# Optimization experiments

Measured on AMD Instinct MI355X. Metric: run time of the kernel, lower is better.

## Reference

```python
import jax, jax.numpy as jnp
import numpy as np

N = 50000
E = 600000
F_IN = 128
HID = 128
N_CLS = 16


def setup_inputs() -> dict:
    key = jax.random.key(0)
    ks = jax.random.split(key, 12)
    x = jax.random.normal(ks[0], (N, F_IN), dtype=jnp.float32)
    edge_index = jax.random.randint(ks[1], (2, E), 0, N, dtype=jnp.int64)
    def glorot(k, shape):
        lim = float(np.sqrt(6.0 / (shape[0] + shape[1])))
        return jax.random.uniform(k, shape, jnp.float32, -lim, lim)
    return {
        "x": x,
        "edge_index": edge_index,
        "W1": glorot(ks[2], (F_IN, HID)), "b1": jnp.zeros((HID,), jnp.float32),
        "W2": glorot(ks[3], (HID, HID)), "b2": jnp.zeros((HID,), jnp.float32),
        "W3": glorot(ks[4], (HID, HID)), "b3": jnp.zeros((HID,), jnp.float32),
        "Wlin": glorot(ks[5], (HID, N_CLS)), "blin": jnp.zeros((N_CLS,), jnp.float32),
    }


def _gcn_norm(edge_index, n_nodes):
    # PyG GCNConv default: add self-loops, symmetric normalization
    loops = jnp.arange(n_nodes, dtype=edge_index.dtype)
    src = jnp.concatenate([edge_index[0], loops])  # [E+N]
    dst = jnp.concatenate([edge_index[1], loops])  # [E+N]
    deg = jax.ops.segment_sum(jnp.ones_like(dst, dtype=jnp.float32), dst,
                              num_segments=n_nodes)
    dis = jnp.where(deg > 0, jax.lax.rsqrt(jnp.maximum(deg, 1.0)), 0.0)
    norm = dis[src] * dis[dst]  # [E+N]
    return src, dst, norm


def _gcn_conv(h, src, dst, norm, n_nodes, W, b):
    h = h @ W                                   # transform first (small GEMM)
    msg = h[src] * norm[:, None]                # gather + scale, [E+N, HID]
    out = jax.ops.segment_sum(msg, dst, num_segments=n_nodes)  # scatter-add
    return out + b


def reference(x, edge_index, W1, b1, W2, b2, W3, b3, Wlin, blin):
    n_nodes = x.shape[0]
    src, dst, norm = _gcn_norm(edge_index, n_nodes)
    h = jax.nn.relu(_gcn_conv(x, src, dst, norm, n_nodes, W1, b1))
    h = jax.nn.relu(_gcn_conv(h, src, dst, norm, n_nodes, W2, b2))
    h = _gcn_conv(h, src, dst, norm, n_nodes, W3, b3)
    return h @ Wlin + blin  # [N, N_CLS]
```

## Files before the change

### kernel.cpp

```cpp
#include <hip/hip_runtime.h>
#include <hip/hip_fp16.h>


#define FD 128
#define NCLS 16

typedef _Float16 f16x8 __attribute__((ext_vector_type(8)));
typedef float f32x4 __attribute__((ext_vector_type(4)));

__global__ __launch_bounds__(256) void k_init_deg(int* __restrict__ degi, int n) {
  int i = blockIdx.x * 256 + threadIdx.x;
  if (i < n) degi[i] = 1;
}

__global__ __launch_bounds__(256) void k_count(const int* __restrict__ dst,
                                               int* __restrict__ degi, int e) {
  int i = blockIdx.x * 256 + threadIdx.x;
  if (i < e) atomicAdd(&degi[dst[i]], 1);
}

__global__ __launch_bounds__(1024) void k_scanA(const int* __restrict__ degi,
                                                int* __restrict__ ptr,
                                                int* __restrict__ bsum,
                                                float* __restrict__ dis, int n) {
  __shared__ int buf[1024];
  int tid = threadIdx.x;
  int i = blockIdx.x * 1024 + tid;
  int dg = (i < n) ? degi[i] : 1;
  if (i < n) dis[i] = rsqrtf((float)dg);
  int v = (i < n) ? (dg - 1) : 0;
  buf[tid] = v;
  __syncthreads();
  for (int off = 1; off < 1024; off <<= 1) {
    int t = (tid >= off) ? buf[tid - off] : 0;
    __syncthreads();
    buf[tid] += t;
    __syncthreads();
  }
  if (i < n) ptr[i] = buf[tid] - v;
  if (tid == 1023) bsum[blockIdx.x] = buf[1023];
}

__global__ void k_scanB(int* __restrict__ bsum, int nb) {
  if (threadIdx.x == 0 && blockIdx.x == 0) {
    int run = 0;
    for (int b = 0; b < nb; ++b) { int t = bsum[b]; bsum[b] = run; run += t; }
  }
}

__global__ __launch_bounds__(256) void k_scanC(int* __restrict__ ptr,
                                               int* __restrict__ cur,
                                               const int* __restrict__ bsum,
                                               int n, int e) {
  int i = blockIdx.x * 256 + threadIdx.x;
  if (i < n) {
    int p = ptr[i] + bsum[i >> 10];
    ptr[i] = p;
    cur[i] = p;
  }
  if (i == 0) ptr[n] = e;
}

__global__ __launch_bounds__(256) void k_fill(const int* __restrict__ src,
                                              const int* __restrict__ dst,
                                              int* __restrict__ cur,
                                              const float* __restrict__ dis,
                                              int2* __restrict__ sn, int e) {
  int i = blockIdx.x * 256 + threadIdx.x;
  if (i < e) {
    int s = src[i], d = dst[i];
    int p = atomicAdd(&cur[d], 1);
    sn[p] = make_int2(s, __float_as_int(dis[s] * dis[d]));
  }
}

__global__ __launch_bounds__(256) void k_convW3(const float* __restrict__ W1,
                                                const float* __restrict__ W2,
                                                const float* __restrict__ W3,
                                                __half* __restrict__ wp) {
  int gi = blockIdx.x * 256 + threadIdx.x;
  int which = gi >> 14;
  int i = gi & 16383;
  const float* W = (which == 0) ? W1 : ((which == 1) ? W2 : W3);
  int j = i & 7;
  int l = (i >> 3) & 63;
  int kc = (i >> 9) & 3;
  int c = i >> 11;
  int k = kc * 32 + ((l >> 4) << 3) + j;
  int col = c * 16 + (l & 15);
  wp[gi] = __float2half_rn(W[k * FD + col]);
}

__global__ __launch_bounds__(256) void k_gemm_mfma(const void* __restrict__ Ain,
                                                   int a_fp32,
                                                   const __half* __restrict__ Wp,
                                                   __half* __restrict__ C, int n) {
  __shared__ uint4 al4[1024];
  __shared__ uint4 wl4[2048];
  int tid = threadIdx.x;
  const uint4* wsrc = reinterpret_cast<const uint4*>(Wp);
  for (int i = tid; i < 2048; i += 256) wl4[i] = wsrc[i];

  int rb = blockIdx.x * 64;
  if (a_fp32) {
    const float* A = (const float*)Ain;
    for (int i = tid; i < 2048; i += 256) {
      int row = i >> 5, seg = i & 31;
      int g = rb + row;
      if (g > n - 1) g = n - 1;
      float4 v = *reinterpret_cast<const float4*>(A + (size_t)g * FD + seg * 4);
      __half h[4];
      h[0] = __float2half_rn(v.x); h[1] = __float2half_rn(v.y);
      h[2] = __float2half_rn(v.z); h[3] = __float2half_rn(v.w);
      *reinterpret_cast<uint2*>(reinterpret_cast<char*>(al4) + row * 256 +
                                ((seg * 8) ^ ((row & 7) << 4))) =
          *reinterpret_cast<uint2*>(h);
    }
  } else {
    const __half* A = (const __half*)Ain;
    for (int i = tid; i < 1024; i += 256) {
      int row = i >> 4, b = (i & 15) << 4;
      int g = rb + row;
      if (g > n - 1) g = n - 1;
      uint4 v = *reinterpret_cast<const uint4*>(
          reinterpret_cast<const char*>(A) + (size_t)g * 256 + b);
      *reinterpret_cast<uint4*>(reinterpret_cast<char*>(al4) + row * 256 +
                                (b ^ ((row & 7) << 4))) = v;
    }
  }
  __syncthreads();

  int l = tid & 63, wid = tid >> 6;
  int arow = wid * 16 + (l & 15);
  f16x8 af[4];
#pragma unroll
  for (int kc = 0; kc < 4; ++kc) {
    int b = kc * 64 + ((l >> 4) << 4);
    af[kc] = *reinterpret_cast<const f16x8*>(
        reinterpret_cast<const char*>(al4) + arow * 256 + (b ^ ((arow & 7) << 4)));
  }

  const __half* wl = reinterpret_cast<const __half*>(wl4);
  f32x4 acc[8];
#pragma unroll
  for (int c = 0; c < 8; ++c) acc[c] = (f32x4){0.f, 0.f, 0.f, 0.f};
#pragma unroll
  for (int c = 0; c < 8; ++c) {
#pragma unroll
    for (int kc = 0; kc < 4; ++kc) {
      f16x8 bf = *reinterpret_cast<const f16x8*>(&wl[((c * 4 + kc) * 64 + l) * 8]);
      acc[c] = __builtin_amdgcn_mfma_f32_16x16x32_f16(af[kc], bf, acc[c], 0, 0, 0);
    }
  }

  __syncthreads();
  {
    char* cl = reinterpret_cast<char*>(al4);
    int crow0 = wid * 16 + ((l >> 4) << 2);
#pragma unroll
    for (int c = 0; c < 8; ++c) {
      int colb = (c * 16 + (l & 15)) * 2;
#pragma unroll
      for (int r = 0; r < 4; ++r) {
        int row = crow0 + r;
        *reinterpret_cast<__half*>(cl + row * 256 + (colb ^ ((row & 7) << 4))) =
            __float2half_rn(acc[c][r]);
      }
    }
  }
  __syncthreads();
  for (int i = tid; i < 1024; i += 256) {
    int row = i >> 4, seg = i & 15;
    int g = rb + row;
    if (g < n)
      *reinterpret_cast<uint4*>(reinterpret_cast<char*>(C) + (size_t)g * 256 +
                                seg * 16) =
          *reinterpret_cast<const uint4*>(reinterpret_cast<const char*>(al4) +
                                          row * 256 +
                                          ((seg * 16) ^ ((row & 7) << 4)));
  }
}

__device__ __forceinline__ void agg_wave(const __half* __restrict__ t,
                                         const int* __restrict__ ptr,
                                         const int2* __restrict__ sn,
                                         int node, int lane, float o[4]) {
  int h = lane >> 5;
  int q = lane & 31;
  float a0 = 0.f, a1 = 0.f, a2 = 0.f, a3 = 0.f;
  int e0 = ptr[node], e1 = ptr[node + 1];
  for (int base = e0; base < e1; base += 16) {
    int s[8];
    float w[8];
#pragma unroll
    for (int j = 0; j < 8; ++j) {
      int idx = base + 2 * j + h;
      if (idx < e1) {
        int2 p = sn[idx];
        s[j] = p.x;
        w[j] = __int_as_float(p.y);
      } else {
        s[j] = node;
        w[j] = 0.f;
      }
    }
    ushort4 v[8];
#pragma unroll
    for (int j = 0; j < 8; ++j)
      v[j] = *reinterpret_cast<const ushort4*>(&t[(size_t)s[j] * FD + q * 4]);
#pragma unroll
    for (int j = 0; j < 8; ++j) {
      a0 = fmaf(__half2float(__ushort_as_half(v[j].x)), w[j], a0);
      a1 = fmaf(__half2float(__ushort_as_half(v[j].y)), w[j], a1);
      a2 = fmaf(__half2float(__ushort_as_half(v[j].z)), w[j], a2);
      a3 = fmaf(__half2float(__ushort_as_half(v[j].w)), w[j], a3);
    }
  }
  o[0] = a0 + __shfl(a0, lane ^ 32, 64);
  o[1] = a1 + __shfl(a1, lane ^ 32, 64);
  o[2] = a2 + __shfl(a2, lane ^ 32, 64);
  o[3] = a3 + __shfl(a3, lane ^ 32, 64);
}

template <int SELF>
__global__ __launch_bounds__(256) void k_probe(const __half* __restrict__ t,
                                               const int* __restrict__ ptr,
                                               const int2* __restrict__ sn,
                                               float* __restrict__ pr) {
  int lane = threadIdx.x & 63;
  int node = blockIdx.x * 4 + (threadIdx.x >> 6);
  int h = lane >> 5, q = lane & 31;
  float a0 = 0.f, a1 = 0.f, a2 = 0.f, a3 = 0.f;
  int e0 = ptr[node], e1 = ptr[node + 1];
  for (int base = e0; base < e1; base += 16) {
    int s[8];
    float w[8];
#pragma unroll
    for (int j = 0; j < 8; ++j) {
      int idx = base + 2 * j + h;
      if (idx < e1) {
        int2 p = sn[idx];
        s[j] = p.x;
        w[j] = __int_as_float(p.y);
      } else {
        s[j] = node;
        w[j] = 0.f;
      }
      if (SELF) {
        int nd = node;
        asm volatile("" : "+v"(nd));
        s[j] = nd;
      }
    }
    ushort4 v[8];
#pragma unroll
    for (int j = 0; j < 8; ++j)
      v[j] = *reinterpret_cast<const ushort4*>(&t[(size_t)s[j] * FD + q * 4]);
#pragma unroll
    for (int j = 0; j < 8; ++j) {
      a0 = fmaf(__half2float(__ushort_as_half(v[j].x)), w[j], a0);
      a1 = fmaf(__half2float(__ushort_as_half(v[j].y)), w[j], a1);
      a2 = fmaf(__half2float(__ushort_as_half(v[j].z)), w[j], a2);
      a3 = fmaf(__half2float(__ushort_as_half(v[j].w)), w[j], a3);
    }
  }
  a0 += __shfl(a0, lane ^ 32, 64);
  a1 += __shfl(a1, lane ^ 32, 64);
  a2 += __shfl(a2, lane ^ 32, 64);
  a3 += __shfl(a3, lane ^ 32, 64);
  if (lane < 32)
    *reinterpret_cast<float4*>(&pr[((size_t)node * 32 + q) * 4]) =
        make_float4(a0, a1, a2, a3);
}

__global__ __launch_bounds__(256) void k_agg(const __half* __restrict__ t,
                                             const int* __restrict__ ptr,
                                             const int2* __restrict__ sn,
                                             const float* __restrict__ dis,
                                             const float* __restrict__ bias,
                                             __half* __restrict__ out, int relu) {
  int lane = threadIdx.x & 63;
  int node = blockIdx.x * 4 + (threadIdx.x >> 6);
  float d = dis[node];
  float dd = d * d;
  float o[4];
  agg_wave(t, ptr, sn, node, lane, o);
  if (lane < 32) {
    int q = lane;
    ushort4 sv = *reinterpret_cast<const ushort4*>(&t[(size_t)node * FD + q * 4]);
    float4 b = *reinterpret_cast<const float4*>(&bias[q * 4]);
    o[0] = fmaf(__half2float(__ushort_as_half(sv.x)), dd, o[0]) + b.x;
    o[1] = fmaf(__half2float(__ushort_as_half(sv.y)), dd, o[1]) + b.y;
    o[2] = fmaf(__half2float(__ushort_as_half(sv.z)), dd, o[2]) + b.z;
    o[3] = fmaf(__half2float(__ushort_as_half(sv.w)), dd, o[3]) + b.w;
    if (relu) {
      o[0] = fmaxf(o[0], 0.f);
      o[1] = fmaxf(o[1], 0.f);
      o[2] = fmaxf(o[2], 0.f);
      o[3] = fmaxf(o[3], 0.f);
    }
    __half hh[4];
    hh[0] = __float2half_rn(o[0]);
    hh[1] = __float2half_rn(o[1]);
    hh[2] = __float2half_rn(o[2]);
    hh[3] = __float2half_rn(o[3]);
    *reinterpret_cast<uint2*>(&out[(size_t)node * FD + q * 4]) =
        *reinterpret_cast<uint2*>(hh);
  }
}

__global__ __launch_bounds__(256) void k_agg_lin(const __half* __restrict__ t,
                                                 const int* __restrict__ ptr,
                                                 const int2* __restrict__ sn,
                                                 const float* __restrict__ dis,
                                                 const float* __restrict__ b3,
                                                 const float* __restrict__ Wl,
                                                 const float* __restrict__ bl,
                                                 float* __restrict__ out) {
  __shared__ float hl[4][FD];
  int wid = threadIdx.x >> 6;
  int lane = threadIdx.x & 63;
  int node = blockIdx.x * 4 + wid;
  float d = dis[node];
  float dd = d * d;
  float o[4];
  agg_wave(t, ptr, sn, node, lane, o);
  if (lane < 32) {
    int q = lane;
    ushort4 sv = *reinterpret_cast<const ushort4*>(&t[(size_t)node * FD + q * 4]);
    float4 b = *reinterpret_cast<const float4*>(&b3[q * 4]);
    hl[wid][q * 4 + 0] = fmaf(__half2float(__ushort_as_half(sv.x)), dd, o[0]) + b.x;
    hl[wid][q * 4 + 1] = fmaf(__half2float(__ushort_as_half(sv.y)), dd, o[1]) + b.y;
    hl[wid][q * 4 + 2] = fmaf(__half2float(__ushort_as_half(sv.z)), dd, o[2]) + b.z;
    hl[wid][q * 4 + 3] = fmaf(__half2float(__ushort_as_half(sv.w)), dd, o[3]) + b.w;
  }
  __syncthreads();
  int c = lane & 15, kc = lane >> 4;
  float s = 0.f;
#pragma unroll
  for (int k0 = 0; k0 < 32; ++k0) {
    int k = kc * 32 + k0;
    s = fmaf(hl[wid][k], Wl[k * NCLS + c], s);
  }
  s += __shfl(s, lane ^ 16, 64);
  s += __shfl(s, lane ^ 32, 64);
  if (lane < NCLS)
    out[(size_t)node * NCLS + lane] = s + bl[lane];
}

extern "C" void kernel_launch(void* const* d_in, const int* in_sizes, int n_in,
                              void* d_out, int out_size, void* d_ws, size_t ws_size,
                              hipStream_t stream) {
  const float* x  = (const float*)d_in[0];
  const int*   ei = (const int*)d_in[1];
  const float* W1 = (const float*)d_in[2];
  const float* b1 = (const float*)d_in[3];
  const float* W2 = (const float*)d_in[4];
  const float* b2 = (const float*)d_in[5];
  const float* W3 = (const float*)d_in[6];
  const float* b3 = (const float*)d_in[7];
  const float* Wl = (const float*)d_in[8];
  const float* bl = (const float*)d_in[9];
  float* out = (float*)d_out;

  const int n = in_sizes[0] / FD;
  const int e = in_sizes[1] / 2;
  const int* src = ei;
  const int* dst = ei + e;

  __half* thA = (__half*)d_ws;
  __half* thB = thA + (size_t)n * FD;
  float*  pr  = (float*)(thB + (size_t)n * FD);
  __half* wp1 = (__half*)(pr + (size_t)n * FD);
  __half* wp2 = wp1 + 16384;
  __half* wp3 = wp2 + 16384;
  int*   degi = (int*)(wp3 + 16384);
  float* dis  = (float*)(degi + n);
  int*   ptr  = (int*)(dis + n);
  int*   cur  = ptr + n + 1;
  int*   bsum = cur + n;
  int2*  sn   = (int2*)(((uintptr_t)(bsum + 64) + 15) & ~(uintptr_t)15);

  const int gn = (n + 255) / 256;
  const int ge = (e + 255) / 256;
  const int nb = (n + 1023) / 1024;

  k_init_deg<<<gn, 256, 0, stream>>>(degi, n);
  k_count<<<ge, 256, 0, stream>>>(dst, degi, e);
  k_scanA<<<nb, 1024, 0, stream>>>(degi, ptr, bsum, dis, n);
  k_scanB<<<1, 64, 0, stream>>>(bsum, nb);
  k_scanC<<<gn, 256, 0, stream>>>(ptr, cur, bsum, n, e);
  k_fill<<<ge, 256, 0, stream>>>(src, dst, cur, dis, sn, e);
  k_convW3<<<192, 256, 0, stream>>>(W1, W2, W3, wp1);

  const int gG = (n + 63) / 64;
  const int ga = n / 4;

  k_gemm_mfma<<<gG, 256, 0, stream>>>(x, 1, wp1, thA, n);
  k_agg<<<ga, 256, 0, stream>>>(thA, ptr, sn, dis, b1, thB, 1);
  k_gemm_mfma<<<gG, 256, 0, stream>>>(thB, 0, wp2, thA, n);
  k_agg<<<ga, 256, 0, stream>>>(thA, ptr, sn, dis, b2, thB, 1);
  k_gemm_mfma<<<gG, 256, 0, stream>>>(thB, 0, wp3, thA, n);
  k_agg_lin<<<ga, 256, 0, stream>>>(thA, ptr, sn, dis, b3, Wl, bl, out);

  k_probe<1><<<ga, 256, 0, stream>>>(thA, ptr, sn, pr);
}
```

Baseline: 336.3 us.

## Fold W3 into classifier, drop probe kernel, use grid-stride aggregation

Removes the leftover probe kernel, which was pure extra work. Uses linearity to precompute W3·Wlin and b3·Wlin+blin, so the third layer aggregates the 128-wide hidden state and projects straight to 16 classes, skipping the third GEMM. The aggregation kernels become grid-stride loops over a fixed grid of 2048 blocks. It adds a small single-block kernel for the weight product, and the third layer now aggregates layer-2 output directly, which changes the rounding order.

```diff
diff --git a/kernel.cpp b/kernel.cpp
--- a/kernel.cpp
+++ b/kernel.cpp
@@ -74,14 +74,13 @@
   }
 }
 
-__global__ __launch_bounds__(256) void k_convW3(const float* __restrict__ W1,
+__global__ __launch_bounds__(256) void k_convW2(const float* __restrict__ W1,
                                                 const float* __restrict__ W2,
-                                                const float* __restrict__ W3,
                                                 __half* __restrict__ wp) {
   int gi = blockIdx.x * 256 + threadIdx.x;
   int which = gi >> 14;
   int i = gi & 16383;
-  const float* W = (which == 0) ? W1 : ((which == 1) ? W2 : W3);
+  const float* W = (which == 0) ? W1 : W2;
   int j = i & 7;
   int l = (i >> 3) & 63;
   int kc = (i >> 9) & 3;
@@ -89,6 +88,29 @@
   int k = kc * 32 + ((l >> 4) << 3) + j;
   int col = c * 16 + (l & 15);
   wp[gi] = __float2half_rn(W[k * FD + col]);
+}
+
+__global__ __launch_bounds__(256) void k_fuse3(const float* __restrict__ W3,
+                                               const float* __restrict__ Wl,
+                                               const float* __restrict__ b3,
+                                               const float* __restrict__ bl,
+                                               float* __restrict__ W3p,
+                                               float* __restrict__ b3p) {
+  int tid = threadIdx.x;
+  for (int i = tid; i < FD * NCLS; i += 256) {
+    int k = i >> 4, c = i & 15;
+    float s = 0.f;
+#pragma unroll 8
+    for (int m = 0; m < FD; ++m)
+      s = fmaf(W3[k * FD + m], Wl[m * NCLS + c], s);
+    W3p[i] = s;
+  }
+  if (tid < NCLS) {
+    float s = bl[tid];
+    for (int m = 0; m < FD; ++m)
+      s = fmaf(b3[m], Wl[m * NCLS + tid], s);
+    b3p[tid] = s;
+  }
 }
 
 __global__ __launch_bounds__(256) void k_gemm_mfma(const void* __restrict__ Ain,
@@ -222,90 +244,45 @@
   o[3] = a3 + __shfl(a3, lane ^ 32, 64);
 }
 
-template <int SELF>
-__global__ __launch_bounds__(256) void k_probe(const __half* __restrict__ t,
-                                               const int* __restrict__ ptr,
-                                               const int2* __restrict__ sn,
-                                               float* __restrict__ pr) {
-  int lane = threadIdx.x & 63;
-  int node = blockIdx.x * 4 + (threadIdx.x >> 6);
-  int h = lane >> 5, q = lane & 31;
-  float a0 = 0.f, a1 = 0.f, a2 = 0.f, a3 = 0.f;
-  int e0 = ptr[node], e1 = ptr[node + 1];
-  for (int base = e0; base < e1; base += 16) {
-    int s[8];
-    float w[8];
-#pragma unroll
-    for (int j = 0; j < 8; ++j) {
-      int idx = base + 2 * j + h;
-      if (idx < e1) {
-        int2 p = sn[idx];
-        s[j] = p.x;
-        w[j] = __int_as_float(p.y);
-      } else {
-        s[j] = node;
-        w[j] = 0.f;
-      }
-      if (SELF) {
-        int nd = node;
-        asm volatile("" : "+v"(nd));
-        s[j] = nd;
-      }
-    }
-    ushort4 v[8];
-#pragma unroll
-    for (int j = 0; j < 8; ++j)
-      v[j] = *reinterpret_cast<const ushort4*>(&t[(size_t)s[j] * FD + q * 4]);
-#pragma unroll
-    for (int j = 0; j < 8; ++j) {
-      a0 = fmaf(__half2float(__ushort_as_half(v[j].x)), w[j], a0);
-      a1 = fmaf(__half2float(__ushort_as_half(v[j].y)), w[j], a1);
-      a2 = fmaf(__half2float(__ushort_as_half(v[j].z)), w[j], a2);
-      a3 = fmaf(__half2float(__ushort_as_half(v[j].w)), w[j], a3);
-    }
-  }
-  a0 += __shfl(a0, lane ^ 32, 64);
-  a1 += __shfl(a1, lane ^ 32, 64);
-  a2 += __shfl(a2, lane ^ 32, 64);
-  a3 += __shfl(a3, lane ^ 32, 64);
-  if (lane < 32)
-    *reinterpret_cast<float4*>(&pr[((size_t)node * 32 + q) * 4]) =
-        make_float4(a0, a1, a2, a3);
-}
-
 __global__ __launch_bounds__(256) void k_agg(const __half* __restrict__ t,
                                              const int* __restrict__ ptr,
                                              const int2* __restrict__ sn,
                                              const float* __restrict__ dis,
                                              const float* __restrict__ bias,
-                                             __half* __restrict__ out, int relu) {
+                                             __half* __restrict__ out, int relu,
+                                             int n) {
   int lane = threadIdx.x & 63;
-  int node = blockIdx.x * 4 + (threadIdx.x >> 6);
-  float d = dis[node];
-  float dd = d * d;
-  float o[4];
-  agg_wave(t, ptr, sn, node, lane, o);
-  if (lane < 32) {
-    int q = lane;
-    ushort4 sv = *reinterpret_cast<const ushort4*>(&t[(size_t)node * FD + q * 4]);
-    float4 b = *reinterpret_cast<const float4*>(&bias[q * 4]);
-    o[0] = fmaf(__half2float(__ushort_as_half(sv.x)), dd, o[0]) + b.x;
-    o[1] = fmaf(__half2float(__ushort_as_half(sv.y)), dd, o[1]) + b.y;
-    o[2] = fmaf(__half2float(__ushort_as_half(sv.z)), dd, o[2]) + b.z;
-    o[3] = fmaf(__half2float(__ushort_as_half(sv.w)), dd, o[3]) + b.w;
-    if (relu) {
-      o[0] = fmaxf(o[0], 0.f);
-      o[1] = fmaxf(o[1], 0.f);
-      o[2] = fmaxf(o[2], 0.f);
-      o[3] = fmaxf(o[3], 0.f);
-    }
-    __half hh[4];
-    hh[0] = __float2half_rn(o[0]);
-    hh[1] = __float2half_rn(o[1]);
-    hh[2] = __float2half_rn(o[2]);
-    hh[3] = __float2half_rn(o[3]);
-    *reinterpret_cast<uint2*>(&out[(size_t)node * FD + q * 4]) =
-        *reinterpret_cast<uint2*>(hh);
+  int wid = threadIdx.x >> 6;
+  int stride = gridDim.x * 4;
+  for (int node0 = blockIdx.x * 4; node0 < n; node0 += stride) {
+    int node = node0 + wid;
+    float d = dis[node];
+    float dd = d * d;
+    float o[4];
+    agg_wave(t, ptr, sn, node, lane, o);
+    if (lane < 32) {
+      int q = lane;
+      ushort4 sv =
+          *reinterpret_cast<const ushort4*>(&t[(size_t)node * FD + q * 4]);
+      float4 b = *reinterpret_cast<const float4*>(&bias[q * 4]);
+      o[0] = fmaf(__half2float(__ushort_as_half(sv.x)), dd, o[0]) + b.x;
+      o[1] = fmaf(__half2float(__ushort_as_half(sv.y)), dd, o[1]) + b.y;
+      o[2] = fmaf(__half2float(__ushort_as_half(sv.z)), dd, o[2]) + b.z;
+      o[3] = fmaf(__half2float(__ushort_as_half(sv.w)), dd, o[3]) + b.w;
+      if (relu) {
+        o[0] = fmaxf(o[0], 0.f);
+        o[1] = fmaxf(o[1], 0.f);
+        o[2] = fmaxf(o[2], 0.f);
+        o[3] = fmaxf(o[3], 0.f);
+      }
+      __half hh[4];
+      hh[0] = __float2half_rn(o[0]);
+      hh[1] = __float2half_rn(o[1]);
+      hh[2] = __float2half_rn(o[2]);
+      hh[3] = __float2half_rn(o[3]);
+      *reinterpret_cast<uint2*>(&out[(size_t)node * FD + q * 4]) =
+          *reinterpret_cast<uint2*>(hh);
+    }
   }
 }
 
@@ -313,39 +290,42 @@
                                                  const int* __restrict__ ptr,
                                                  const int2* __restrict__ sn,
                                                  const float* __restrict__ dis,
-                                                 const float* __restrict__ b3,
-                                                 const float* __restrict__ Wl,
-                                                 const float* __restrict__ bl,
-                                                 float* __restrict__ out) {
+                                                 const float* __restrict__ W3p,
+                                                 const float* __restrict__ b3p,
+                                                 float* __restrict__ out, int n) {
   __shared__ float hl[4][FD];
   int wid = threadIdx.x >> 6;
   int lane = threadIdx.x & 63;
-  int node = blockIdx.x * 4 + wid;
-  float d = dis[node];
-  float dd = d * d;
-  float o[4];
-  agg_wave(t, ptr, sn, node, lane, o);
-  if (lane < 32) {
-    int q = lane;
-    ushort4 sv = *reinterpret_cast<const ushort4*>(&t[(size_t)node * FD + q * 4]);
-    float4 b = *reinterpret_cast<const float4*>(&b3[q * 4]);
-    hl[wid][q * 4 + 0] = fmaf(__half2float(__ushort_as_half(sv.x)), dd, o[0]) + b.x;
-    hl[wid][q * 4 + 1] = fmaf(__half2float(__ushort_as_half(sv.y)), dd, o[1]) + b.y;
-    hl[wid][q * 4 + 2] = fmaf(__half2float(__ushort_as_half(sv.z)), dd, o[2]) + b.z;
-    hl[wid][q * 4 + 3] = fmaf(__half2float(__ushort_as_half(sv.w)), dd, o[3]) + b.w;
-  }
-  __syncthreads();
-  int c = lane & 15, kc = lane >> 4;
-  float s = 0.f;
-#pragma unroll
-  for (int k0 = 0; k0 < 32; ++k0) {
-    int k = kc * 32 + k0;
-    s = fmaf(hl[wid][k], Wl[k * NCLS + c], s);
-  }
-  s += __shfl(s, lane ^ 16, 64);
-  s += __shfl(s, lane ^ 32, 64);
-  if (lane < NCLS)
-    out[(size_t)node * NCLS + lane] = s + bl[lane];
+  int stride = gridDim.x * 4;
+  for (int node0 = blockIdx.x * 4; node0 < n; node0 += stride) {
+    int node = node0 + wid;
+    float d = dis[node];
+    float dd = d * d;
+    float o[4];
+    agg_wave(t, ptr, sn, node, lane, o);
+    if (lane < 32) {
+      int q = lane;
+      ushort4 sv =
+          *reinterpret_cast<const ushort4*>(&t[(size_t)node * FD + q * 4]);
+      hl[wid][q * 4 + 0] = fmaf(__half2float(__ushort_as_half(sv.x)), dd, o[0]);
+      hl[wid][q * 4 + 1] = fmaf(__half2float(__ushort_as_half(sv.y)), dd, o[1]);
+      hl[wid][q * 4 + 2] = fmaf(__half2float(__ushort_as_half(sv.z)), dd, o[2]);
+      hl[wid][q * 4 + 3] = fmaf(__half2float(__ushort_as_half(sv.w)), dd, o[3]);
+    }
+    __syncthreads();
+    int c = lane & 15, kc = lane >> 4;
+    float s = 0.f;
+#pragma unroll
+    for (int k0 = 0; k0 < 32; ++k0) {
+      int k = kc * 32 + k0;
+      s = fmaf(hl[wid][k], W3p[k * NCLS + c], s);
+    }
+    s += __shfl(s, lane ^ 16, 64);
+    s += __shfl(s, lane ^ 32, 64);
+    if (lane < NCLS)
+      out[(size_t)node * NCLS + lane] = s + b3p[lane];
+    __syncthreads();
+  }
 }
 
 extern "C" void kernel_launch(void* const* d_in, const int* in_sizes, int n_in,
@@ -370,11 +350,11 @@
 
   __half* thA = (__half*)d_ws;
   __half* thB = thA + (size_t)n * FD;
-  float*  pr  = (float*)(thB + (size_t)n * FD);
-  __half* wp1 = (__half*)(pr + (size_t)n * FD);
+  __half* wp1 = thB + (size_t)n * FD;
   __half* wp2 = wp1 + 16384;
-  __half* wp3 = wp2 + 16384;
-  int*   degi = (int*)(wp3 + 16384);
+  float*  W3p = (float*)(wp2 + 16384);
+  float*  b3p = W3p + 2048;
+  int*   degi = (int*)(b3p + 16);
   float* dis  = (float*)(degi + n);
   int*   ptr  = (int*)(dis + n);
   int*   cur  = ptr + n + 1;
@@ -391,17 +371,15 @@
   k_scanB<<<1, 64, 0, stream>>>(bsum, nb);
   k_scanC<<<gn, 256, 0, stream>>>(ptr, cur, bsum, n, e);
   k_fill<<<ge, 256, 0, stream>>>(src, dst, cur, dis, sn, e);
-  k_convW3<<<192, 256, 0, stream>>>(W1, W2, W3, wp1);
+  k_convW2<<<128, 256, 0, stream>>>(W1, W2, wp1);
+  k_fuse3<<<1, 256, 0, stream>>>(W3, Wl, b3, bl, W3p, b3p);
 
   const int gG = (n + 63) / 64;
-  const int ga = n / 4;
+  const int ga = 2048;
 
   k_gemm_mfma<<<gG, 256, 0, stream>>>(x, 1, wp1, thA, n);
-  k_agg<<<ga, 256, 0, stream>>>(thA, ptr, sn, dis, b1, thB, 1);
+  k_agg<<<ga, 256, 0, stream>>>(thA, ptr, sn, dis, b1, thB, 1, n);
   k_gemm_mfma<<<gG, 256, 0, stream>>>(thB, 0, wp2, thA, n);
-  k_agg<<<ga, 256, 0, stream>>>(thA, ptr, sn, dis, b2, thB, 1);
-  k_gemm_mfma<<<gG, 256, 0, stream>>>(thB, 0, wp3, thA, n);
-  k_agg_lin<<<ga, 256, 0, stream>>>(thA, ptr, sn, dis, b3, Wl, bl, out);
-
-  k_probe<1><<<ga, 256, 0, stream>>>(thA, ptr, sn, pr);
-}
+  k_agg<<<ga, 256, 0, stream>>>(thA, ptr, sn, dis, b2, thB, 1, n);
+  k_agg_lin<<<ga, 256, 0, stream>>>(thB, ptr, sn, dis, W3p, b3p, out, n);
+}
```

Result: no change. 333.7 us (-0.8%).
